# Kernel tuning notes

Measured on AMD Instinct MI355X. Metric: run time of the kernel, lower is better.

Reference implementation:

```python
import jax, jax.numpy as jnp
import numpy as np

N = 50000
E = 1600000
IN_DIM = 128
HID = 64


def setup_inputs() -> dict:
    key = jax.random.key(0)
    ks = jax.random.split(key, 8)
    x = jax.random.normal(ks[0], (N, IN_DIM), dtype=jnp.float32)
    edge_row = jax.random.randint(ks[1], (E,), 0, N, dtype=jnp.int32)
    edge_col = jax.random.randint(ks[2], (E,), 0, N, dtype=jnp.int32)
    edge_val = jax.random.uniform(ks[3], (E,), dtype=jnp.float32)
    W1 = jax.random.normal(ks[4], (IN_DIM, HID), dtype=jnp.float32) * (1.0 / np.sqrt(IN_DIM))
    b1 = jnp.zeros((HID,), dtype=jnp.float32)
    W2 = jax.random.normal(ks[5], (HID, 1), dtype=jnp.float32) * (1.0 / np.sqrt(HID))
    b2 = jnp.zeros((1,), dtype=jnp.float32)
    return {"x": x, "edge_row": edge_row, "edge_col": edge_col,
            "edge_val": edge_val, "W1": W1, "b1": b1, "W2": W2, "b2": b2}


def reference(x, edge_row, edge_col, edge_val, W1, b1, W2, b2):
    # h = tanh(x @ W1 + b1)  -> [N, HID]
    h = jnp.tanh(x @ W1 + b1)
    # sparse adjacency matmul: out[i] = sum_{e: row[e]==i} val[e] * h[col[e]]
    gathered = edge_val[:, None] * h[edge_col]            # [E, HID]
    agg = jax.ops.segment_sum(gathered, edge_row, num_segments=N)  # [N, HID]
    # final linear projection to scalar per node
    return agg @ W2 + b2                                   # [N, 1]
```

## Files before the change

kernel.cpp:

```cpp
#include <hip/hip_runtime.h>

#define IN_DIM 128
#define HID 64
#define SHIFT 7
#define RPB 128
#define NBPAD 512
#define CAP 6144
#define SBLK 256

__global__ __launch_bounds__(256) void node_kernel(
    const float* __restrict__ x, const float* __restrict__ W1,
    const float* __restrict__ b1, const float* __restrict__ W2,
    float* __restrict__ g, int n, int* __restrict__ gcnt)
{
    __shared__ float sx[64][IN_DIM];
    __shared__ float sw[IN_DIM][HID];
    if (blockIdx.x == 0)
        for (int i = threadIdx.x; i < NBPAD; i += 256) gcnt[i] = 0;

    const int node0 = blockIdx.x * 64;

    {
        const float4* src = reinterpret_cast<const float4*>(W1);
        float4* dst = reinterpret_cast<float4*>(&sw[0][0]);
        for (int i = threadIdx.x; i < (IN_DIM * HID) / 4; i += 256) dst[i] = src[i];
    }
    for (int i = threadIdx.x; i < (64 * IN_DIM) / 4; i += 256) {
        int f  = i * 4;
        int nd = f >> 7;
        int k  = f & (IN_DIM - 1);
        int gn = min(node0 + nd, n - 1);
        *reinterpret_cast<float4*>(&sx[nd][k]) =
            *reinterpret_cast<const float4*>(x + (size_t)gn * IN_DIM + k);
    }
    __syncthreads();

    const int tx = threadIdx.x & 15;
    const int ty = threadIdx.x >> 4;

    float acc[4][4];
    #pragma unroll
    for (int j = 0; j < 4; ++j) {
        float bj = b1[tx * 4 + j];
        #pragma unroll
        for (int i = 0; i < 4; ++i) acc[i][j] = bj;
    }

    #pragma unroll 2
    for (int k = 0; k < IN_DIM; k += 4) {
        float4 xa[4], wb[4];
        #pragma unroll
        for (int i = 0; i < 4; ++i)
            xa[i] = *reinterpret_cast<const float4*>(&sx[ty * 4 + i][k]);
        #pragma unroll
        for (int j = 0; j < 4; ++j)
            wb[j] = *reinterpret_cast<const float4*>(&sw[k + j][tx * 4]);
        #pragma unroll
        for (int i = 0; i < 4; ++i) {
            acc[i][0] += xa[i].x * wb[0].x; acc[i][1] += xa[i].x * wb[0].y;
            acc[i][2] += xa[i].x * wb[0].z; acc[i][3] += xa[i].x * wb[0].w;
            acc[i][0] += xa[i].y * wb[1].x; acc[i][1] += xa[i].y * wb[1].y;
            acc[i][2] += xa[i].y * wb[1].z; acc[i][3] += xa[i].y * wb[1].w;
            acc[i][0] += xa[i].z * wb[2].x; acc[i][1] += xa[i].z * wb[2].y;
            acc[i][2] += xa[i].z * wb[2].z; acc[i][3] += xa[i].z * wb[2].w;
            acc[i][0] += xa[i].w * wb[3].x; acc[i][1] += xa[i].w * wb[3].y;
            acc[i][2] += xa[i].w * wb[3].z; acc[i][3] += xa[i].w * wb[3].w;
        }
    }

    float w2v[4];
    #pragma unroll
    for (int j = 0; j < 4; ++j) w2v[j] = W2[tx * 4 + j];
    #pragma unroll
    for (int i = 0; i < 4; ++i) {
        float s = 0.f;
        #pragma unroll
        for (int j = 0; j < 4; ++j) {
            float a = fminf(fmaxf(acc[i][j], -15.f), 15.f);
            float ex = __expf(2.f * a);
            s += ((ex - 1.f) / (ex + 1.f)) * w2v[j];
        }
        #pragma unroll
        for (int off = 1; off < 16; off <<= 1) s += __shfl_xor(s, off);
        if (tx == 0) {
            int nd = node0 + ty * 4 + i;
            if (nd < n) g[nd] = s;
        }
    }
}

__global__ __launch_bounds__(256) void scatter_kernel(
    const int* __restrict__ erow, const int* __restrict__ ecol,
    const float* __restrict__ ev, int e, int chunk,
    int* __restrict__ gcnt, uint2* __restrict__ pairs)
{
    __shared__ int h[NBPAD];
    __shared__ int cur[NBPAD];
    for (int i = threadIdx.x; i < NBPAD; i += 256) h[i] = 0;
    __syncthreads();
    const int s = blockIdx.x * chunk, t = min(e, s + chunk);
    const int cnt = t - s, cnt4 = cnt >> 2;

    const int4*   r4 = reinterpret_cast<const int4*>(erow + s);
    const int4*   c4 = reinterpret_cast<const int4*>(ecol + s);
    const float4* v4 = reinterpret_cast<const float4*>(ev + s);

    for (int i = threadIdx.x; i < cnt4; i += 256) {
        int4 r = r4[i];
        atomicAdd(&h[r.x >> SHIFT], 1);
        atomicAdd(&h[r.y >> SHIFT], 1);
        atomicAdd(&h[r.z >> SHIFT], 1);
        atomicAdd(&h[r.w >> SHIFT], 1);
    }
    for (int i = s + (cnt4 << 2) + threadIdx.x; i < t; i += 256)
        atomicAdd(&h[erow[i] >> SHIFT], 1);
    __syncthreads();
    for (int b = threadIdx.x; b < NBPAD; b += 256)
        cur[b] = h[b] ? atomicAdd(&gcnt[b], h[b]) : 0;
    __syncthreads();

    for (int i = threadIdx.x; i < cnt4; i += 256) {
        int4 r = r4[i]; int4 c = c4[i]; float4 v = v4[i];
        {
            int b = r.x >> SHIFT; int pos = atomicAdd(&cur[b], 1);
            if (pos < CAP) pairs[(size_t)b * CAP + pos] =
                make_uint2(((unsigned)(r.x & (RPB-1)) << 16) | (unsigned)c.x, __float_as_uint(v.x));
        }
        {
            int b = r.y >> SHIFT; int pos = atomicAdd(&cur[b], 1);
            if (pos < CAP) pairs[(size_t)b * CAP + pos] =
                make_uint2(((unsigned)(r.y & (RPB-1)) << 16) | (unsigned)c.y, __float_as_uint(v.y));
        }
        {
            int b = r.z >> SHIFT; int pos = atomicAdd(&cur[b], 1);
            if (pos < CAP) pairs[(size_t)b * CAP + pos] =
                make_uint2(((unsigned)(r.z & (RPB-1)) << 16) | (unsigned)c.z, __float_as_uint(v.z));
        }
        {
            int b = r.w >> SHIFT; int pos = atomicAdd(&cur[b], 1);
            if (pos < CAP) pairs[(size_t)b * CAP + pos] =
                make_uint2(((unsigned)(r.w & (RPB-1)) << 16) | (unsigned)c.w, __float_as_uint(v.w));
        }
    }
    for (int i = s + (cnt4 << 2) + threadIdx.x; i < t; i += 256) {
        int r = erow[i];
        int b = r >> SHIFT; int pos = atomicAdd(&cur[b], 1);
        if (pos < CAP) pairs[(size_t)b * CAP + pos] =
            make_uint2(((unsigned)(r & (RPB-1)) << 16) | (unsigned)ecol[i], __float_as_uint(ev[i]));
    }
}

__global__ __launch_bounds__(256) void reduce_kernel(
    const uint2* __restrict__ pairs, const int* __restrict__ gcnt,
    const float* __restrict__ g, const float* __restrict__ b2,
    float* __restrict__ out, int n)
{
    __shared__ float acc[RPB];
    const int b = blockIdx.x;
    for (int i = threadIdx.x; i < RPB; i += 256) acc[i] = 0.f;
    __syncthreads();
    const int m = min(gcnt[b], CAP);
    const uint2* p = pairs + (size_t)b * CAP;
    const uint4* p4 = reinterpret_cast<const uint4*>(p);
    const int nq = m >> 2;
    for (int i = threadIdx.x; i < nq; i += 256) {
        uint4 a = p4[2 * i];
        uint4 c = p4[2 * i + 1];
        float g0 = g[a.x & 0xFFFF], g1 = g[a.z & 0xFFFF];
        float g2 = g[c.x & 0xFFFF], g3 = g[c.z & 0xFFFF];
        atomicAdd(&acc[(a.x >> 16) & (RPB-1)], __uint_as_float(a.y) * g0);
        atomicAdd(&acc[(a.z >> 16) & (RPB-1)], __uint_as_float(a.w) * g1);
        atomicAdd(&acc[(c.x >> 16) & (RPB-1)], __uint_as_float(c.y) * g2);
        atomicAdd(&acc[(c.z >> 16) & (RPB-1)], __uint_as_float(c.w) * g3);
    }
    for (int i = (nq << 2) + threadIdx.x; i < m; i += 256) {
        uint2 eu = p[i];
        atomicAdd(&acc[(eu.x >> 16) & (RPB-1)], __uint_as_float(eu.y) * g[eu.x & 0xFFFF]);
    }
    __syncthreads();
    const float bias = b2[0];
    const int row0 = b << SHIFT;
    for (int i = threadIdx.x; i < RPB; i += 256) {
        int r = row0 + i;
        if (r < n) out[r] = acc[i] + bias;
    }
}

extern "C" void kernel_launch(void* const* d_in, const int* in_sizes, int n_in,
                              void* d_out, int out_size, void* d_ws, size_t ws_size,
                              hipStream_t stream) {
    const float* x    = (const float*)d_in[0];
    const int*   erow = (const int*)  d_in[1];
    const int*   ecol = (const int*)  d_in[2];
    const float* ev   = (const float*)d_in[3];
    const float* W1   = (const float*)d_in[4];
    const float* b1   = (const float*)d_in[5];
    const float* W2   = (const float*)d_in[6];
    const float* b2   = (const float*)d_in[7];
    float* out = (float*)d_out;

    const int n  = in_sizes[0] / IN_DIM;
    const int e  = in_sizes[1];
    const int nb = (n + RPB - 1) >> SHIFT;

    char* ws = (char*)d_ws;
    float* g = (float*)ws;
    size_t off = ((size_t)n * 4 + 255) & ~(size_t)255;
    int* gcnt = (int*)(ws + off); off += NBPAD * 4;
    uint2* pairs = (uint2*)(ws + off);

    const int chunk = (((e + SBLK - 1) / SBLK) + 3) & ~3;

    node_kernel   <<<(n + 63) / 64, 256, 0, stream>>>(x, W1, b1, W2, g, n, gcnt);
    scatter_kernel<<<SBLK, 256, 0, stream>>>(erow, ecol, ev, e, chunk, gcnt, pairs);
    reduce_kernel <<<nb, 256, 0, stream>>>(pairs, gcnt, g, b2, out, n);
}
```

Measured before the change: 142.1 us.

## Split per-bucket reduction into segments and widen scatter blocks

```diff
diff --git a/kernel.cpp b/kernel.cpp
--- a/kernel.cpp
+++ b/kernel.cpp
@@ -7,6 +7,7 @@
 #define NBPAD 512
 #define CAP 6144
 #define SBLK 256
+#define NSEG 4
 
 __global__ __launch_bounds__(256) void node_kernel(
     const float* __restrict__ x, const float* __restrict__ W1,
@@ -89,14 +90,14 @@
     }
 }
 
-__global__ __launch_bounds__(256) void scatter_kernel(
+__global__ __launch_bounds__(1024) void scatter_kernel(
     const int* __restrict__ erow, const int* __restrict__ ecol,
     const float* __restrict__ ev, int e, int chunk,
     int* __restrict__ gcnt, uint2* __restrict__ pairs)
 {
     __shared__ int h[NBPAD];
     __shared__ int cur[NBPAD];
-    for (int i = threadIdx.x; i < NBPAD; i += 256) h[i] = 0;
+    for (int i = threadIdx.x; i < NBPAD; i += 1024) h[i] = 0;
     __syncthreads();
     const int s = blockIdx.x * chunk, t = min(e, s + chunk);
     const int cnt = t - s, cnt4 = cnt >> 2;
@@ -105,21 +106,21 @@
     const int4*   c4 = reinterpret_cast<const int4*>(ecol + s);
     const float4* v4 = reinterpret_cast<const float4*>(ev + s);
 
-    for (int i = threadIdx.x; i < cnt4; i += 256) {
+    for (int i = threadIdx.x; i < cnt4; i += 1024) {
         int4 r = r4[i];
         atomicAdd(&h[r.x >> SHIFT], 1);
         atomicAdd(&h[r.y >> SHIFT], 1);
         atomicAdd(&h[r.z >> SHIFT], 1);
         atomicAdd(&h[r.w >> SHIFT], 1);
     }
-    for (int i = s + (cnt4 << 2) + threadIdx.x; i < t; i += 256)
+    for (int i = s + (cnt4 << 2) + threadIdx.x; i < t; i += 1024)
         atomicAdd(&h[erow[i] >> SHIFT], 1);
     __syncthreads();
-    for (int b = threadIdx.x; b < NBPAD; b += 256)
+    for (int b = threadIdx.x; b < NBPAD; b += 1024)
         cur[b] = h[b] ? atomicAdd(&gcnt[b], h[b]) : 0;
     __syncthreads();
 
-    for (int i = threadIdx.x; i < cnt4; i += 256) {
+    for (int i = threadIdx.x; i < cnt4; i += 1024) {
         int4 r = r4[i]; int4 c = c4[i]; float4 v = v4[i];
         {
             int b = r.x >> SHIFT; int pos = atomicAdd(&cur[b], 1);
@@ -142,7 +143,7 @@
                 make_uint2(((unsigned)(r.w & (RPB-1)) << 16) | (unsigned)c.w, __float_as_uint(v.w));
         }
     }
-    for (int i = s + (cnt4 << 2) + threadIdx.x; i < t; i += 256) {
+    for (int i = s + (cnt4 << 2) + threadIdx.x; i < t; i += 1024) {
         int r = erow[i];
         int b = r >> SHIFT; int pos = atomicAdd(&cur[b], 1);
         if (pos < CAP) pairs[(size_t)b * CAP + pos] =
@@ -152,38 +153,46 @@
 
 __global__ __launch_bounds__(256) void reduce_kernel(
     const uint2* __restrict__ pairs, const int* __restrict__ gcnt,
-    const float* __restrict__ g, const float* __restrict__ b2,
+    const float* __restrict__ g, float* __restrict__ partial)
+{
+    __shared__ float acc[RPB];
+    const int b   = blockIdx.x >> 2;
+    const int seg = blockIdx.x & (NSEG - 1);
+    for (int i = threadIdx.x; i < RPB; i += 256) acc[i] = 0.f;
+    __syncthreads();
+    const int m  = min(gcnt[b], CAP);
+    const int s0 = (m * seg)       >> 2;
+    const int s1 = (m * (seg + 1)) >> 2;
+    const uint2* p = pairs + (size_t)b * CAP;
+
+    int i = s0 + (int)threadIdx.x;
+    for (; i + 768 < s1; i += 1024) {
+        uint2 e0 = p[i], e1 = p[i + 256], e2 = p[i + 512], e3 = p[i + 768];
+        float g0 = g[e0.x & 0xFFFF], g1 = g[e1.x & 0xFFFF];
+        float g2 = g[e2.x & 0xFFFF], g3 = g[e3.x & 0xFFFF];
+        atomicAdd(&acc[e0.x >> 16], __uint_as_float(e0.y) * g0);
+        atomicAdd(&acc[e1.x >> 16], __uint_as_float(e1.y) * g1);
+        atomicAdd(&acc[e2.x >> 16], __uint_as_float(e2.y) * g2);
+        atomicAdd(&acc[e3.x >> 16], __uint_as_float(e3.y) * g3);
+    }
+    for (; i < s1; i += 256) {
+        uint2 eu = p[i];
+        atomicAdd(&acc[eu.x >> 16], __uint_as_float(eu.y) * g[eu.x & 0xFFFF]);
+    }
+    __syncthreads();
+    float* pp = partial + (size_t)blockIdx.x * RPB;
+    for (int k = threadIdx.x; k < RPB; k += 256) pp[k] = acc[k];
+}
+
+__global__ __launch_bounds__(256) void combine_kernel(
+    const float* __restrict__ partial, const float* __restrict__ b2,
     float* __restrict__ out, int n)
 {
-    __shared__ float acc[RPB];
-    const int b = blockIdx.x;
-    for (int i = threadIdx.x; i < RPB; i += 256) acc[i] = 0.f;
-    __syncthreads();
-    const int m = min(gcnt[b], CAP);
-    const uint2* p = pairs + (size_t)b * CAP;
-    const uint4* p4 = reinterpret_cast<const uint4*>(p);
-    const int nq = m >> 2;
-    for (int i = threadIdx.x; i < nq; i += 256) {
-        uint4 a = p4[2 * i];
-        uint4 c = p4[2 * i + 1];
-        float g0 = g[a.x & 0xFFFF], g1 = g[a.z & 0xFFFF];
-        float g2 = g[c.x & 0xFFFF], g3 = g[c.z & 0xFFFF];
-        atomicAdd(&acc[(a.x >> 16) & (RPB-1)], __uint_as_float(a.y) * g0);
-        atomicAdd(&acc[(a.z >> 16) & (RPB-1)], __uint_as_float(a.w) * g1);
-        atomicAdd(&acc[(c.x >> 16) & (RPB-1)], __uint_as_float(c.y) * g2);
-        atomicAdd(&acc[(c.z >> 16) & (RPB-1)], __uint_as_float(c.w) * g3);
-    }
-    for (int i = (nq << 2) + threadIdx.x; i < m; i += 256) {
-        uint2 eu = p[i];
-        atomicAdd(&acc[(eu.x >> 16) & (RPB-1)], __uint_as_float(eu.y) * g[eu.x & 0xFFFF]);
-    }
-    __syncthreads();
-    const float bias = b2[0];
-    const int row0 = b << SHIFT;
-    for (int i = threadIdx.x; i < RPB; i += 256) {
-        int r = row0 + i;
-        if (r < n) out[r] = acc[i] + bias;
-    }
+    const int r = blockIdx.x * 256 + threadIdx.x;
+    if (r >= n) return;
+    const int b = r >> SHIFT, rl = r & (RPB - 1);
+    const float* pp = partial + ((size_t)b * NSEG) * RPB + rl;
+    out[r] = pp[0] + pp[RPB] + pp[2 * RPB] + pp[3 * RPB] + b2[0];
 }
 
 extern "C" void kernel_launch(void* const* d_in, const int* in_sizes, int n_in,
@@ -207,11 +216,13 @@
     float* g = (float*)ws;
     size_t off = ((size_t)n * 4 + 255) & ~(size_t)255;
     int* gcnt = (int*)(ws + off); off += NBPAD * 4;
+    float* partial = (float*)(ws + off); off += (size_t)NBPAD * NSEG * RPB * 4;
     uint2* pairs = (uint2*)(ws + off);
 
     const int chunk = (((e + SBLK - 1) / SBLK) + 3) & ~3;
 
     node_kernel   <<<(n + 63) / 64, 256, 0, stream>>>(x, W1, b1, W2, g, n, gcnt);
-    scatter_kernel<<<SBLK, 256, 0, stream>>>(erow, ecol, ev, e, chunk, gcnt, pairs);
-    reduce_kernel <<<nb, 256, 0, stream>>>(pairs, gcnt, g, b2, out, n);
-}
+    scatter_kernel<<<SBLK, 1024, 0, stream>>>(erow, ecol, ev, e, chunk, gcnt, pairs);
+    reduce_kernel <<<nb * NSEG, 256, 0, stream>>>(pairs, gcnt, g, partial);
+    combine_kernel<<<(n + 255) / 256, 256, 0, stream>>>(partial, b2, out, n);
+}
```

New measurement: 137.9 us. -2.9%, faster.
